# Optimization experiments

Measured on AMD Instinct MI355X. Metric: run time of the kernel, lower is better.

## Reference

```python
import jax, jax.numpy as jnp
import numpy as np
import math

D = 256; H = 8; DH = 32; FF = 2048; L = 6; B = 4; S = 1022


def _pe(n, d):
    pos = np.arange(n)[:, None]
    div = np.exp(np.arange(0, d, 2) * (-math.log(10000.0) / d))
    pe = np.zeros((n, d), np.float32)
    pe[:, 0::2] = np.sin(pos * div)
    pe[:, 1::2] = np.cos(pos * div)
    return jnp.asarray(pe)


def _ln(x, g, b):
    mu = x.mean(-1, keepdims=True)
    v = ((x - mu) ** 2).mean(-1, keepdims=True)
    return (x - mu) / jnp.sqrt(v + 1e-5) * g + b


def _forward(x, cls1, cls2, Wqkv, bqkv, Wo, bo, ln1_g, ln1_b, W1, b1, W2, b2, ln2_g, ln2_b, idx, pad):
    n = x.shape[1] + 2  # insert cls1 and cls2 tokens
    h = jnp.stack([jnp.concatenate([cls1, x[i, :idx[i]], cls2, x[i, idx[i]:]], axis=0) for i in range(B)])
    h = h + _pe(n, D)[None]  # [B,N,D]
    # block-diagonal two-segment mask per sample (additive bias form)
    pos = np.arange(n)
    bias = []
    for i in range(B):
        v1 = pos <= idx[i]
        v2 = (pos > idx[i]) & (pos < n - pad[i])
        allowed = np.outer(v1, v1) | np.outer(v2, v2)
        bias.append(np.where(allowed, 0.0, -1e9).astype(np.float32))
    bias = jnp.asarray(np.stack(bias))[:, None]  # [B,1,N,N]
    scale = 1.0 / math.sqrt(DH)
    for l in range(L):
        qkv = h @ Wqkv[l].T + bqkv[l]  # [B,N,3D]
        q, k, v = jnp.split(qkv, 3, axis=-1)
        q = q.reshape(B, n, H, DH).transpose(0, 2, 1, 3)
        k = k.reshape(B, n, H, DH).transpose(0, 2, 1, 3)
        v = v.reshape(B, n, H, DH).transpose(0, 2, 1, 3)
        scores = jnp.einsum('bhqd,bhkd->bhqk', q, k) * scale + bias
        p = jax.nn.softmax(scores, axis=-1)
        a = jnp.einsum('bhqk,bhkd->bhqd', p, v).transpose(0, 2, 1, 3).reshape(B, n, D)
        h = _ln(h + a @ Wo[l].T + bo[l], ln1_g[l], ln1_b[l])
        ff = jax.nn.relu(h @ W1[l].T + b1[l]) @ W2[l].T + b2[l]
        h = _ln(h + ff, ln2_g[l], ln2_b[l])
    # cls token outputs: position 0 (cls1) and position idx+1 (cls2)
    return jnp.stack([jnp.stack([h[i, 0], h[i, idx[i] + 1]]) for i in range(B)])  # [4,2,256]


def setup_inputs():
    key = jax.random.key(0)
    ks = jax.random.split(key, 8)
    s = 0.02
    return {
        'x': jax.random.normal(ks[0], (B, S, D), jnp.float32),
        'mask': jnp.zeros((1,), jnp.bool_),  # unused by the original forward
        'indices': jnp.array([[500, 600, 400, 300], [0, 0, 0, 0]], jnp.int32),
        'cls1': jax.random.uniform(ks[1], (1, D), jnp.float32),
        'cls2': jax.random.uniform(ks[2], (1, D), jnp.float32),
        'Wqkv': jax.random.normal(ks[3], (L, 3 * D, D), jnp.float32) * s,
        'bqkv': jnp.zeros((L, 3 * D), jnp.float32),
        'Wo': jax.random.normal(ks[4], (L, D, D), jnp.float32) * s,
        'bo': jnp.zeros((L, D), jnp.float32),
        'ln1_g': jnp.ones((L, D), jnp.float32),
        'ln1_b': jnp.zeros((L, D), jnp.float32),
        'W1': jax.random.normal(ks[5], (L, FF, D), jnp.float32) * s,
        'b1': jnp.zeros((L, FF), jnp.float32),
        'W2': jax.random.normal(ks[6], (L, D, FF), jnp.float32) * s,
        'b2': jnp.zeros((L, D), jnp.float32),
        'ln2_g': jnp.ones((L, D), jnp.float32),
        'ln2_b': jnp.zeros((L, D), jnp.float32),
    }


def reference(x, mask, indices, cls1, cls2, Wqkv, bqkv, Wo, bo, ln1_g, ln1_b, W1, b1, W2, b2, ln2_g, ln2_b):
    ind = np.asarray(indices)
    idx = [int(t) for t in ind[0]]
    pad = [int(t) for t in ind[1]]
    return _forward(x, cls1, cls2, Wqkv, bqkv, Wo, bo, ln1_g, ln1_b, W1, b1, W2, b2, ln2_g, ln2_b, idx, pad)
```

## Files before the change

kernel.cpp:

```cpp
#include <hip/hip_runtime.h>
#include <hip/hip_bf16.h>
#include <math.h>

typedef __hip_bfloat16 bf16;
typedef short bf16x8 __attribute__((ext_vector_type(8)));
typedef short short4v __attribute__((ext_vector_type(4)));
typedef float f32x4 __attribute__((ext_vector_type(4)));

#define D_MODEL 256
#define NTOK 1024
#define SEQ 1022
#define BATCH 4
#define NLAYER 6

__device__ inline void gload_lds16(const void* g, void* l) {
    __builtin_amdgcn_global_load_lds(
        (const __attribute__((address_space(1))) void*)g,
        (__attribute__((address_space(3))) void*)l, 16, 0, 0);
}

__global__ __launch_bounds__(256) void cast4_kernel(
    const float* __restrict__ s0, bf16* __restrict__ d0,
    const float* __restrict__ s1, bf16* __restrict__ d1,
    const float* __restrict__ s2, bf16* __restrict__ d2,
    const float* __restrict__ s3, bf16* __restrict__ d3)
{
    const int bid = blockIdx.x;
    const float* s; bf16* d; int base;
    if (bid < 1152)      { s = s0; d = d0; base = bid; }
    else if (bid < 1536) { s = s1; d = d1; base = bid - 1152; }
    else if (bid < 4608) { s = s2; d = d2; base = bid - 1536; }
    else                 { s = s3; d = d3; base = bid - 4608; }
    const int i = (base * 256 + threadIdx.x) * 4;
    f32x4 v = *(const f32x4*)(s + i);
    d[i + 0] = __float2bfloat16(v[0]);
    d[i + 1] = __float2bfloat16(v[1]);
    d[i + 2] = __float2bfloat16(v[2]);
    d[i + 3] = __float2bfloat16(v[3]);
}

__global__ __launch_bounds__(256) void embed_kernel(
    const float* __restrict__ x, const float* __restrict__ cls1,
    const float* __restrict__ cls2, const int* __restrict__ ind,
    float* __restrict__ h, bf16* __restrict__ hb)
{
    int i = blockIdx.x * 256 + threadIdx.x;
    int d = i & 255;
    int pos = (i >> 8) & 1023;
    int b = i >> 18;
    int idx = ind[b];
    float v;
    if (pos == 0) v = cls1[d];
    else if (pos == idx + 1) v = cls2[d];
    else if (pos <= idx) v = x[(b * SEQ + pos - 1) * D_MODEL + d];
    else v = x[(b * SEQ + pos - 2) * D_MODEL + d];
    int p = d >> 1;
    float freq = expf(-(float)p * (logf(10000.0f) / 128.0f));
    float ang = (float)pos * freq;
    v += (d & 1) ? cosf(ang) : sinf(ang);
    h[i] = v;
    hb[i] = __float2bfloat16(v);
}

template<int MR, int NR, int RELU, int HAS_RES, int WF32, int WBF16, int WVT>
__global__ __launch_bounds__(256) void mfma_gemm(
    const bf16* __restrict__ A, const bf16* __restrict__ W,
    const float* __restrict__ bias, const float* __restrict__ R,
    float* __restrict__ Cf, bf16* __restrict__ Cb, bf16* __restrict__ vTb,
    int M, int N, int K)
{
    constexpr int BM = MR * 32, BN = NR * 32;
    constexpr int ACH = BM * 4;
    constexpr int BCH = BN * 4;
    __shared__ bf16 As[2][BM * 32];
    __shared__ bf16 Bs[2][BN * 32];
    const int ntile = N / BN;
    const int bx = blockIdx.x % ntile, by = blockIdx.x / ntile;
    const int row0 = by * BM, col0 = bx * BN;
    const int tid = threadIdx.x, lane = tid & 63, wave = tid >> 6;
    const int wr = wave >> 1, wc = wave & 1;
    const int l15 = lane & 15, l4 = lane >> 4;

    f32x4 acc[MR][NR];
    #pragma unroll
    for (int m = 0; m < MR; ++m)
        #pragma unroll
        for (int n = 0; n < NR; ++n) acc[m][n] = (f32x4)0.0f;

    const int nk = K / 32;

    auto stage = [&](int buf, int t) {
        const int k0 = t * 32;
        #pragma unroll
        for (int p = 0; p < ACH / 256; ++p) {
            const int cbase = p * 256 + wave * 64;
            const int chunk = cbase + lane;
            const int r = chunk >> 2, c = chunk & 3;
            gload_lds16(A + (size_t)(row0 + r) * K + k0 + c * 8, &As[buf][cbase * 8]);
        }
        #pragma unroll
        for (int p = 0; p < BCH / 256; ++p) {
            const int cbase = p * 256 + wave * 64;
            const int chunk = cbase + lane;
            const int r = chunk >> 2, c = chunk & 3;
            gload_lds16(W + (size_t)(col0 + r) * K + k0 + c * 8, &Bs[buf][cbase * 8]);
        }
    };

    stage(0, 0);
    __syncthreads();
    int cur = 0;
    for (int t = 0; t < nk; ++t) {
        if (t + 1 < nk) stage(cur ^ 1, t + 1);
        bf16x8 af[MR], bfr[NR];
        #pragma unroll
        for (int m = 0; m < MR; ++m)
            af[m] = *(const bf16x8*)&As[cur][(wr * MR * 16 + m * 16 + l15) * 32 + l4 * 8];
        #pragma unroll
        for (int n = 0; n < NR; ++n)
            bfr[n] = *(const bf16x8*)&Bs[cur][(wc * NR * 16 + n * 16 + l15) * 32 + l4 * 8];
        #pragma unroll
        for (int m = 0; m < MR; ++m)
            #pragma unroll
            for (int n = 0; n < NR; ++n)
                acc[m][n] = __builtin_amdgcn_mfma_f32_16x16x32_bf16(af[m], bfr[n], acc[m][n], 0, 0, 0);
        __syncthreads();
        cur ^= 1;
    }

    #pragma unroll
    for (int m = 0; m < MR; ++m) {
        #pragma unroll
        for (int n = 0; n < NR; ++n) {
            const int col = col0 + wc * NR * 16 + n * 16 + l15;
            const float bv = bias[col];
            #pragma unroll
            for (int r = 0; r < 4; ++r) {
                const int row = row0 + wr * MR * 16 + m * 16 + l4 * 4 + r;
                float v = acc[m][n][r] + bv;
                if (HAS_RES) v += R[(size_t)row * N + col];
                if (RELU) v = fmaxf(v, 0.0f);
                if (WF32) Cf[(size_t)row * N + col] = v;
                if (WBF16) {
                    if (WVT && col >= 512) {
                        const int hh = (col >> 5) - 16, d = col & 31;
                        const int bb = row >> 10, tt = row & 1023;
                        vTb[(((size_t)bb * 8 + hh) * 32 + d) * 1024 + tt] = __float2bfloat16(v);
                    } else {
                        Cb[(size_t)row * N + col] = __float2bfloat16(v);
                    }
                }
            }
        }
    }
}

template<int K>
__global__ __launch_bounds__(512) void gemm256_ln8_kernel(
    const bf16* __restrict__ A, const bf16* __restrict__ W,
    const float* __restrict__ bias, const float* __restrict__ g,
    const float* __restrict__ be, float* __restrict__ h, bf16* __restrict__ hb)
{
    constexpr int KW = K / 8;
    constexpr int NSTEP = KW / 32;
    __shared__ float part[4][16][260];
    const int tid = threadIdx.x, lane = tid & 63, wave = tid >> 6;
    const int l15 = lane & 15, l4 = lane >> 4;
    const int row0 = blockIdx.x * 16;

    f32x4 acc[16];
    #pragma unroll
    for (int n = 0; n < 16; ++n) acc[n] = (f32x4)0.0f;
    #pragma unroll
    for (int s = 0; s < NSTEP; ++s) {
        const int kk = wave * KW + s * 32;
        const bf16x8 af = *(const bf16x8*)(A + (size_t)(row0 + l15) * K + kk + l4 * 8);
        #pragma unroll
        for (int n = 0; n < 16; ++n) {
            const bf16x8 bfr = *(const bf16x8*)(W + (size_t)(n * 16 + l15) * K + kk + l4 * 8);
            acc[n] = __builtin_amdgcn_mfma_f32_16x16x32_bf16(af, bfr, acc[n], 0, 0, 0);
        }
    }
    if (wave < 4) {
        #pragma unroll
        for (int n = 0; n < 16; ++n)
            #pragma unroll
            for (int r = 0; r < 4; ++r)
                part[wave][l4 * 4 + r][n * 16 + l15] = acc[n][r];
    }
    __syncthreads();
    if (wave >= 4) {
        #pragma unroll
        for (int n = 0; n < 16; ++n)
            #pragma unroll
            for (int r = 0; r < 4; ++r)
                part[wave - 4][l4 * 4 + r][n * 16 + l15] += acc[n][r];
    }
    __syncthreads();

    const int row = tid >> 5, c8 = (tid & 31) * 8;
    f32x4 v0 = *(const f32x4*)&part[0][row][c8];
    f32x4 v1 = *(const f32x4*)&part[0][row][c8 + 4];
    #pragma unroll
    for (int w = 1; w < 4; ++w) {
        v0 += *(const f32x4*)&part[w][row][c8];
        v1 += *(const f32x4*)&part[w][row][c8 + 4];
    }
    float* hrow = h + (size_t)(row0 + row) * 256 + c8;
    v0 += *(const f32x4*)(bias + c8)     + *(const f32x4*)(hrow);
    v1 += *(const f32x4*)(bias + c8 + 4) + *(const f32x4*)(hrow + 4);
    float s1 = (v0[0] + v0[1]) + (v0[2] + v0[3]) + (v1[0] + v1[1]) + (v1[2] + v1[3]);
    #pragma unroll
    for (int off = 16; off >= 1; off >>= 1) s1 += __shfl_xor(s1, off);
    const float mu = s1 * (1.0f / 256.0f);
    float s2 = 0.0f;
    #pragma unroll
    for (int q = 0; q < 4; ++q) { float d0 = v0[q] - mu, d1 = v1[q] - mu; s2 += d0 * d0 + d1 * d1; }
    #pragma unroll
    for (int off = 16; off >= 1; off >>= 1) s2 += __shfl_xor(s2, off);
    const float inv = 1.0f / sqrtf(s2 * (1.0f / 256.0f) + 1e-5f);
    short* hbrow = (short*)hb + (size_t)(row0 + row) * 256 + c8;
    const f32x4 gv0 = *(const f32x4*)(g + c8),  gv1 = *(const f32x4*)(g + c8 + 4);
    const f32x4 ev0 = *(const f32x4*)(be + c8), ev1 = *(const f32x4*)(be + c8 + 4);
    f32x4 y0, y1; short4v p0, p1;
    #pragma unroll
    for (int q = 0; q < 4; ++q) {
        y0[q] = (v0[q] - mu) * inv * gv0[q] + ev0[q];
        y1[q] = (v1[q] - mu) * inv * gv1[q] + ev1[q];
        p0[q] = __builtin_bit_cast(short, __float2bfloat16(y0[q]));
        p1[q] = __builtin_bit_cast(short, __float2bfloat16(y1[q]));
    }
    *(f32x4*)(hrow) = y0;  *(f32x4*)(hrow + 4) = y1;
    *(short4v*)(hbrow) = p0;  *(short4v*)(hbrow + 4) = p1;
}

__global__ __launch_bounds__(256) void ln_kernel(
    const float* __restrict__ X, const float* __restrict__ g,
    const float* __restrict__ bb, float* __restrict__ Y, bf16* __restrict__ Yb)
{
    const int row = blockIdx.x * 4 + (threadIdx.x >> 6);
    const int lane = threadIdx.x & 63;
    const f32x4 xv = *(const f32x4*)(X + (size_t)row * 256 + lane * 4);
    float s = (xv[0] + xv[1]) + (xv[2] + xv[3]);
    #pragma unroll
    for (int off = 32; off >= 1; off >>= 1) s += __shfl_xor(s, off);
    const float mu = s * (1.0f / 256.0f);
    f32x4 dv;
    float s2 = 0.0f;
    #pragma unroll
    for (int e = 0; e < 4; ++e) { dv[e] = xv[e] - mu; s2 += dv[e] * dv[e]; }
    #pragma unroll
    for (int off = 32; off >= 1; off >>= 1) s2 += __shfl_xor(s2, off);
    const float inv = 1.0f / sqrtf(s2 * (1.0f / 256.0f) + 1e-5f);
    const f32x4 gv = *(const f32x4*)(g + lane * 4);
    const f32x4 bv = *(const f32x4*)(bb + lane * 4);
    f32x4 y;
    short4v pk;
    #pragma unroll
    for (int e = 0; e < 4; ++e) {
        y[e] = dv[e] * inv * gv[e] + bv[e];
        pk[e] = __builtin_bit_cast(short, __float2bfloat16(y[e]));
    }
    *(f32x4*)(Y + (size_t)row * 256 + lane * 4) = y;
    *(short4v*)((short*)Yb + (size_t)row * 256 + lane * 4) = pk;
}

__global__ __launch_bounds__(256) void attn_mfma_kernel(
    const bf16* __restrict__ qkvb, const bf16* __restrict__ vT,
    bf16* __restrict__ att, const int* __restrict__ ind)
{
    __shared__ bf16 Ps[4][16][72];
    const int qt = blockIdx.x & 15;
    const int hh = (blockIdx.x >> 4) & 7;
    const int b  = blockIdx.x >> 7;
    const int idx = ind[b];
    const int segEnd = NTOK - ind[4 + b];
    const int tid = threadIdx.x, lane = tid & 63, wave = tid >> 6;
    const int l15 = lane & 15, l4 = lane >> 4;
    const int q0 = qt * 64 + wave * 16;
    const size_t tokbase = (size_t)b * NTOK;
    const bf16* vTh = vT + (((size_t)b * 8 + hh) * 32) * 1024;
    const float scale = 0.17677669529663687f;

    const bf16x8 qfrag = *(const bf16x8*)(qkvb + (tokbase + q0 + l15) * 768 + hh * 32 + l4 * 8);

    f32x4 acc_o[2];
    acc_o[0] = (f32x4)0.0f; acc_o[1] = (f32x4)0.0f;
    float mrun[4], lrun[4];
    bool v1q[4], v2q[4];
    #pragma unroll
    for (int r = 0; r < 4; ++r) {
        mrun[r] = -1e30f; lrun[r] = 0.0f;
        const int qg = q0 + l4 * 4 + r;
        v1q[r] = (qg <= idx);
        v2q[r] = (qg > idx) && (qg < segEnd);
    }

    const int kbeg = (q0 <= idx) ? 0 : (idx + 1);
    const int kend = (q0 + 15 > idx) ? segEnd : (idx + 1);

    for (int k0 = (kbeg & ~63); k0 < kend; k0 += 64) {
        f32x4 sc[4];
        #pragma unroll
        for (int kt = 0; kt < 4; ++kt) {
            const bf16x8 kf = *(const bf16x8*)
                (qkvb + (tokbase + k0 + kt * 16 + l15) * 768 + 256 + hh * 32 + l4 * 8);
            sc[kt] = __builtin_amdgcn_mfma_f32_16x16x32_bf16(qfrag, kf, (f32x4)0.0f, 0, 0, 0);
        }
        float mloc[4] = {-1e30f, -1e30f, -1e30f, -1e30f};
        #pragma unroll
        for (int kt = 0; kt < 4; ++kt) {
            const int k = k0 + kt * 16 + l15;
            const bool v1k = (k <= idx);
            const bool v2k = (k > idx) && (k < segEnd);
            #pragma unroll
            for (int r = 0; r < 4; ++r) {
                const bool ok = (v1q[r] && v1k) || (v2q[r] && v2k);
                const float s = ok ? sc[kt][r] * scale : -1e30f;
                sc[kt][r] = s;
                mloc[r] = fmaxf(mloc[r], s);
            }
        }
        #pragma unroll
        for (int r = 0; r < 4; ++r) {
            mloc[r] = fmaxf(mloc[r], __shfl_xor(mloc[r], 1));
            mloc[r] = fmaxf(mloc[r], __shfl_xor(mloc[r], 2));
            mloc[r] = fmaxf(mloc[r], __shfl_xor(mloc[r], 4));
            mloc[r] = fmaxf(mloc[r], __shfl_xor(mloc[r], 8));
            const float mnew = fmaxf(mrun[r], mloc[r]);
            const float c = __expf(mrun[r] - mnew);
            mrun[r] = mnew;
            mloc[r] = c;
        }
        float psum[4] = {0.0f, 0.0f, 0.0f, 0.0f};
        #pragma unroll
        for (int kt = 0; kt < 4; ++kt) {
            #pragma unroll
            for (int r = 0; r < 4; ++r) {
                const float s = sc[kt][r];
                const float p = (s > -5e29f) ? __expf(s - mrun[r]) : 0.0f;
                psum[r] += p;
                Ps[wave][l4 * 4 + r][kt * 16 + l15] = __float2bfloat16(p);
            }
        }
        #pragma unroll
        for (int r = 0; r < 4; ++r) {
            float ps = psum[r];
            ps += __shfl_xor(ps, 1); ps += __shfl_xor(ps, 2);
            ps += __shfl_xor(ps, 4); ps += __shfl_xor(ps, 8);
            lrun[r] = lrun[r] * mloc[r] + ps;
            acc_o[0][r] *= mloc[r];
            acc_o[1][r] *= mloc[r];
        }
        #pragma unroll
        for (int ks = 0; ks < 2; ++ks) {
            const bf16x8 pa = *(const bf16x8*)&Ps[wave][l15][ks * 32 + l4 * 8];
            #pragma unroll
            for (int dt = 0; dt < 2; ++dt) {
                const bf16x8 vb = *(const bf16x8*)
                    (vTh + (size_t)(dt * 16 + l15) * 1024 + k0 + ks * 32 + l4 * 8);
                acc_o[dt] = __builtin_amdgcn_mfma_f32_16x16x32_bf16(pa, vb, acc_o[dt], 0, 0, 0);
            }
        }
    }

    #pragma unroll
    for (int r = 0; r < 4; ++r) {
        const float invl = (lrun[r] > 0.0f) ? (1.0f / lrun[r]) : 0.0f;
        const int qg = q0 + l4 * 4 + r;
        bf16* op = att + (tokbase + qg) * 256 + hh * 32 + l15;
        op[0]  = __float2bfloat16(acc_o[0][r] * invl);
        op[16] = __float2bfloat16(acc_o[1][r] * invl);
    }
}

__global__ __launch_bounds__(256) void gather_kernel(
    const float* __restrict__ h, const int* __restrict__ ind, float* __restrict__ out)
{
    int b = blockIdx.x;
    int tid = threadIdx.x;
    out[(b * 2 + 0) * 256 + tid] = h[(b * NTOK + 0) * 256 + tid];
    out[(b * 2 + 1) * 256 + tid] = h[(b * NTOK + ind[b] + 1) * 256 + tid];
}

extern "C" void kernel_launch(void* const* d_in, const int* in_sizes, int n_in,
                              void* d_out, int out_size, void* d_ws, size_t ws_size,
                              hipStream_t stream)
{
    const float* x    = (const float*)d_in[0];
    const int*   ind  = (const int*)d_in[2];
    const float* cls1 = (const float*)d_in[3];
    const float* cls2 = (const float*)d_in[4];
    const float* Wqkv = (const float*)d_in[5];
    const float* bqkv = (const float*)d_in[6];
    const float* Wo   = (const float*)d_in[7];
    const float* bo   = (const float*)d_in[8];
    const float* g1   = (const float*)d_in[9];
    const float* be1  = (const float*)d_in[10];
    const float* W1   = (const float*)d_in[11];
    const float* bf1  = (const float*)d_in[12];
    const float* W2   = (const float*)d_in[13];
    const float* bf2  = (const float*)d_in[14];
    const float* g2   = (const float*)d_in[15];
    const float* be2  = (const float*)d_in[16];
    float* out = (float*)d_out;

    float* ws   = (float*)d_ws;
    float* h    = ws;
    float* tmp  = h + 1048576;
    bf16* hb    = (bf16*)(tmp + 1048576);
    bf16* qkvb  = hb + 1048576;
    bf16* vTb   = qkvb + 3145728;
    bf16* attb  = vTb + 1048576;
    bf16* ffb   = attb + 1048576;
    bf16* wqkvb = ffb + 8388608;
    bf16* wob   = wqkvb + 1179648;
    bf16* w1b   = wob + 393216;
    bf16* w2b   = w1b + 3145728;

    const int M = BATCH * NTOK;

    cast4_kernel<<<7680, 256, 0, stream>>>(Wqkv, wqkvb, Wo, wob, W1, w1b, W2, w2b);
    embed_kernel<<<M, 256, 0, stream>>>(x, cls1, cls2, ind, h, hb);

    for (int l = 0; l < NLAYER; ++l) {
        const bf16*  Wqkv_l = wqkvb + (size_t)l * 196608;
        const float* bqkv_l = bqkv + (size_t)l * 768;
        const bf16*  Wo_l   = wob + (size_t)l * 65536;
        const float* bo_l   = bo + (size_t)l * 256;
        const float* g1_l   = g1 + (size_t)l * 256;
        const float* be1_l  = be1 + (size_t)l * 256;
        const bf16*  W1_l   = w1b + (size_t)l * 524288;
        const float* b1_l   = bf1 + (size_t)l * 2048;
        const bf16*  W2_l   = w2b + (size_t)l * 524288;
        const float* b2_l   = bf2 + (size_t)l * 256;
        const float* g2_l   = g2 + (size_t)l * 256;
        const float* be2_l  = be2 + (size_t)l * 256;

        mfma_gemm<2, 4, 0, 0, 0, 1, 1><<<(M / 64) * (768 / 128), 256, 0, stream>>>(
            hb, Wqkv_l, bqkv_l, nullptr, nullptr, qkvb, vTb, M, 768, 256);
        attn_mfma_kernel<<<BATCH * 8 * 16, 256, 0, stream>>>(qkvb, vTb, attb, ind);
        gemm256_ln8_kernel<256><<<M / 16, 512, 0, stream>>>(
            attb, Wo_l, bo_l, g1_l, be1_l, h, hb);
        mfma_gemm<2, 4, 1, 0, 0, 1, 0><<<(M / 64) * (2048 / 128), 256, 0, stream>>>(
            hb, W1_l, b1_l, nullptr, nullptr, ffb, nullptr, M, 2048, 256);
        mfma_gemm<2, 2, 0, 1, 1, 0, 0><<<(M / 64) * (256 / 64), 256, 0, stream>>>(
            ffb, W2_l, b2_l, h, tmp, nullptr, nullptr, M, 256, 2048);
        ln_kernel<<<M / 4, 256, 0, stream>>>(tmp, g2_l, be2_l, h, hb);
    }

    gather_kernel<<<BATCH, 256, 0, stream>>>(h, ind, out);
}
```

Before: 546.9 us.

## Split attention key range across wave pairs and enlarge FFN1 GEMM tile

The attention kernel now gives each 16-query strip to two waves, each covering half of the key tiles. Their partial online-softmax states are merged through shared memory with a rescale step. This doubles the block count and shortens each wave's serial loop, at the cost of extra LDS traffic and a block-wide barrier. Separately, the FFN1 GEMM uses a 128-row tile, which halves its grid and raises per-block reuse of the weights.

```diff
diff --git a/kernel.cpp b/kernel.cpp
--- a/kernel.cpp
+++ b/kernel.cpp
@@ -270,14 +270,17 @@
     bf16* __restrict__ att, const int* __restrict__ ind)
 {
     __shared__ bf16 Ps[4][16][72];
-    const int qt = blockIdx.x & 15;
-    const int hh = (blockIdx.x >> 4) & 7;
-    const int b  = blockIdx.x >> 7;
+    __shared__ float Opart[4][64][8];
+    __shared__ float MLpart[4][64][8];
+    const int qt = blockIdx.x & 31;
+    const int hh = (blockIdx.x >> 5) & 7;
+    const int b  = blockIdx.x >> 8;
     const int idx = ind[b];
     const int segEnd = NTOK - ind[4 + b];
     const int tid = threadIdx.x, lane = tid & 63, wave = tid >> 6;
+    const int strip = wave >> 1, kh = wave & 1;
     const int l15 = lane & 15, l4 = lane >> 4;
-    const int q0 = qt * 64 + wave * 16;
+    const int q0 = qt * 32 + strip * 16;
     const size_t tokbase = (size_t)b * NTOK;
     const bf16* vTh = vT + (((size_t)b * 8 + hh) * 32) * 1024;
     const float scale = 0.17677669529663687f;
@@ -298,8 +301,13 @@
 
     const int kbeg = (q0 <= idx) ? 0 : (idx + 1);
     const int kend = (q0 + 15 > idx) ? segEnd : (idx + 1);
-
-    for (int k0 = (kbeg & ~63); k0 < kend; k0 += 64) {
+    const int t0 = kbeg & ~63;
+    const int T = (kend - t0 + 63) >> 6;
+    const int i0 = kh ? (T >> 1) : 0;
+    const int i1 = kh ? T : (T >> 1);
+
+    for (int i = i0; i < i1; ++i) {
+        const int k0 = t0 + (i << 6);
         f32x4 sc[4];
         #pragma unroll
         for (int kt = 0; kt < 4; ++kt) {
@@ -366,11 +374,29 @@
 
     #pragma unroll
     for (int r = 0; r < 4; ++r) {
-        const float invl = (lrun[r] > 0.0f) ? (1.0f / lrun[r]) : 0.0f;
-        const int qg = q0 + l4 * 4 + r;
-        bf16* op = att + (tokbase + qg) * 256 + hh * 32 + l15;
-        op[0]  = __float2bfloat16(acc_o[0][r] * invl);
-        op[16] = __float2bfloat16(acc_o[1][r] * invl);
+        Opart[wave][lane][r]     = acc_o[0][r];
+        Opart[wave][lane][4 + r] = acc_o[1][r];
+        MLpart[wave][lane][r]     = mrun[r];
+        MLpart[wave][lane][4 + r] = lrun[r];
+    }
+    __syncthreads();
+    if (kh == 0) {
+        #pragma unroll
+        for (int r = 0; r < 4; ++r) {
+            const float m1 = MLpart[wave + 1][lane][r];
+            const float l1 = MLpart[wave + 1][lane][4 + r];
+            const float ms = fmaxf(mrun[r], m1);
+            const float c0 = __expf(mrun[r] - ms);
+            const float c1 = __expf(m1 - ms);
+            const float lt = lrun[r] * c0 + l1 * c1;
+            const float invl = (lt > 0.0f) ? (1.0f / lt) : 0.0f;
+            const float o0 = (acc_o[0][r] * c0 + Opart[wave + 1][lane][r] * c1) * invl;
+            const float o1 = (acc_o[1][r] * c0 + Opart[wave + 1][lane][4 + r] * c1) * invl;
+            const int qg = q0 + l4 * 4 + r;
+            bf16* op = att + (tokbase + qg) * 256 + hh * 32 + l15;
+            op[0]  = __float2bfloat16(o0);
+            op[16] = __float2bfloat16(o1);
+        }
     }
 }
 
@@ -439,10 +465,10 @@
 
         mfma_gemm<2, 4, 0, 0, 0, 1, 1><<<(M / 64) * (768 / 128), 256, 0, stream>>>(
             hb, Wqkv_l, bqkv_l, nullptr, nullptr, qkvb, vTb, M, 768, 256);
-        attn_mfma_kernel<<<BATCH * 8 * 16, 256, 0, stream>>>(qkvb, vTb, attb, ind);
+        attn_mfma_kernel<<<BATCH * 8 * 32, 256, 0, stream>>>(qkvb, vTb, attb, ind);
         gemm256_ln8_kernel<256><<<M / 16, 512, 0, stream>>>(
             attb, Wo_l, bo_l, g1_l, be1_l, h, hb);
-        mfma_gemm<2, 4, 1, 0, 0, 1, 0><<<(M / 64) * (2048 / 128), 256, 0, stream>>>(
+        mfma_gemm<4, 4, 1, 0, 0, 1, 0><<<(M / 128) * (2048 / 128), 256, 0, stream>>>(
             hb, W1_l, b1_l, nullptr, nullptr, ffb, nullptr, M, 2048, 256);
         mfma_gemm<2, 2, 0, 1, 1, 0, 0><<<(M / 64) * (256 / 64), 256, 0, stream>>>(
             ffb, W2_l, b2_l, h, tmp, nullptr, nullptr, M, 256, 2048);
```

Measured after the change: 541.7 us. No clear change (-0.9%).
